# Kernel optimization log

Hardware: AMD Instinct MI355X
Metric: run time of the kernel (lower is better)

Reference implementation:

```python
import jax, jax.numpy as jnp
import numpy as np

DIM = 192
WIN = 7
HEADS = 6
SHIFT = 3
HID = 4 * DIM


def _ln(x, w, b, eps=1e-5):
    m = jnp.mean(x, axis=-1, keepdims=True)
    v = jnp.var(x, axis=-1, keepdims=True)
    return (x - m) * jax.lax.rsqrt(v + eps) * w + b


def setup_inputs() -> dict:
    key = jax.random.key(0)
    ks = jax.random.split(key, 8)
    B, C, H, W = 16, DIM, 56, 56
    s = lambda k, shape, fan: jax.random.normal(k, shape, jnp.float32) * (1.0 / np.sqrt(fan))
    return {
        "x": jax.random.normal(ks[0], (B, C, H, W), jnp.float32),
        "norm1_w": jnp.ones((C,), jnp.float32),
        "norm1_b": jnp.zeros((C,), jnp.float32),
        "qkv_w": s(ks[1], (3 * C, C), C),
        "qkv_b": jnp.zeros((3 * C,), jnp.float32),
        "proj_w": s(ks[2], (C, C), C),
        "proj_b": jnp.zeros((C,), jnp.float32),
        "norm2_w": jnp.ones((C,), jnp.float32),
        "norm2_b": jnp.zeros((C,), jnp.float32),
        "fc1_w": s(ks[3], (HID, C), C),
        "fc1_b": jnp.zeros((HID,), jnp.float32),
        "fc2_w": s(ks[4], (C, HID), HID),
        "fc2_b": jnp.zeros((C,), jnp.float32),
    }


def reference(x, norm1_w, norm1_b, qkv_w, qkv_b, proj_w, proj_b,
              norm2_w, norm2_b, fc1_w, fc1_b, fc2_w, fc2_b):
    B, C, H, W = x.shape
    shift = SHIFT if (H > WIN and W > WIN) else 0
    shortcut = x

    xl = jnp.transpose(x, (0, 2, 3, 1))            # B,H,W,C
    xl = _ln(xl, norm1_w, norm1_b)
    if shift > 0:
        xl = jnp.roll(xl, shift=(-shift, -shift), axis=(1, 2))
    nH, nW = H // WIN, W // WIN
    xw = xl.reshape(B, nH, WIN, nW, WIN, C)
    xw = jnp.transpose(xw, (0, 1, 3, 2, 4, 5)).reshape(-1, WIN * WIN, C)

    # window attention
    Bw, N, _ = xw.shape
    dh = C // HEADS
    qkv = jnp.einsum('bnc,oc->bno', xw, qkv_w) + qkv_b
    qkv = qkv.reshape(Bw, N, 3, HEADS, dh)
    q, k, v = qkv[:, :, 0], qkv[:, :, 1], qkv[:, :, 2]   # Bw,N,H,dh
    scale = dh ** -0.5
    attn = jnp.einsum('bnhd,bmhd->bhnm', q, k) * scale
    attn = jax.nn.softmax(attn, axis=-1)
    out = jnp.einsum('bhnm,bmhd->bnhd', attn, v).reshape(Bw, N, C)
    out = jnp.einsum('bnc,oc->bno', out, proj_w) + proj_b

    # window reverse -> B,H,W,C
    xl = out.reshape(B, nH, nW, WIN, WIN, C)
    xl = jnp.transpose(xl, (0, 1, 3, 2, 4, 5)).reshape(B, H, W, C)
    if shift > 0:
        xl = jnp.roll(xl, shift=(shift, shift), axis=(1, 2))

    # norm2 + MLP (note: original has NO attention residual)
    xl = _ln(xl, norm2_w, norm2_b)
    h = jnp.einsum('bhwc,oc->bhwo', xl, fc1_w) + fc1_b
    h = jax.nn.gelu(h, approximate=False)
    h = jnp.einsum('bhwo,co->bhwc', h, fc2_w) + fc2_b
    return jnp.transpose(h, (0, 3, 1, 2)) + shortcut
```

## Files before the change

### kernel.cpp

```cpp
#include <hip/hip_runtime.h>
#include <hip/hip_bf16.h>

typedef __bf16 bf16_t;
typedef __bf16 bf16x8 __attribute__((ext_vector_type(8)));
typedef float f32x4 __attribute__((ext_vector_type(4)));

#define MFMA16(a, b, c) __builtin_amdgcn_mfma_f32_16x16x32_bf16((a), (b), (c), 0, 0, 0)


__global__ __launch_bounds__(256) void k_cvt(const float* __restrict__ qkvw,
                                             const float* __restrict__ projw,
                                             const float* __restrict__ fc1w,
                                             const float* __restrict__ fc2w,
                                             bf16_t* __restrict__ dst)
{
    int i = blockIdx.x * 256 + threadIdx.x;
    if (i >= 442368) return;
    float v;
    if (i < 110592)      v = qkvw[i];
    else if (i < 147456) v = projw[i - 110592];
    else if (i < 294912) v = fc1w[i - 147456];
    else                 v = fc2w[i - 294912];
    dst[i] = (bf16_t)v;
}

__global__ __launch_bounds__(1024) void k_ln1(const float* __restrict__ x,
                                              const float* __restrict__ gam,
                                              const float* __restrict__ bet,
                                              bf16_t* __restrict__ xw)
{
    __shared__ float tile[56][193];
    __shared__ bf16_t obuf[56 * 192];
    const int bh = blockIdx.x;
    const int b = bh / 56, h = bh % 56;
    const int tid = threadIdx.x;

    {
        const int g = tid >> 4, u = tid & 15;
        const float* xb = x + (long)b * 602112 + (long)h * 56;
        if (u < 14) {
            #pragma unroll
            for (int k = 0; k < 3; ++k) {
                const int c = g + 64 * k;
                float4 v = *(const float4*)(xb + (long)c * 3136 + u * 4);
                tile[u * 4 + 0][c] = v.x;
                tile[u * 4 + 1][c] = v.y;
                tile[u * 4 + 2][c] = v.z;
                tile[u * 4 + 3][c] = v.w;
            }
        }
    }
    __syncthreads();

    const int wave = tid >> 6, lane = tid & 63;
    const float g0 = gam[lane], g1 = gam[lane + 64], g2 = gam[lane + 128];
    const float b0 = bet[lane], b1 = bet[lane + 64], b2 = bet[lane + 128];
    for (int wp = wave; wp < 56; wp += 16) {
        float v0 = tile[wp][lane], v1 = tile[wp][lane + 64], v2 = tile[wp][lane + 128];
        float s = v0 + v1 + v2;
        float sq = v0 * v0 + v1 * v1 + v2 * v2;
        #pragma unroll
        for (int d = 1; d < 64; d <<= 1) { s += __shfl_xor(s, d); sq += __shfl_xor(sq, d); }
        float mean = s * (1.f / 192.f);
        float var  = sq * (1.f / 192.f) - mean * mean;
        float rs = rsqrtf(var + 1e-5f);
        const int wr = (wp + 53) % 56;
        bf16_t* o = obuf + wr * 192;
        o[lane]       = (bf16_t)((v0 - mean) * rs * g0 + b0);
        o[lane + 64]  = (bf16_t)((v1 - mean) * rs * g1 + b1);
        o[lane + 128] = (bf16_t)((v2 - mean) * rs * g2 + b2);
    }
    __syncthreads();

    const int hr = (h + 53) % 56;
    const int nh = hr / 7, ii = hr % 7;
    const long rband = ((long)b * 64 + (long)nh * 8) * 49 + (long)ii * 7;
    const int4* src = (const int4*)obuf;
    for (int q = tid; q < 1344; q += 1024) {
        const int g = q / 168, u = q % 168;
        const int jj = u / 24, ci = u % 24;
        const long r = rband + (long)g * 49 + jj;
        ((int4*)xw)[r * 24 + ci] = src[(g * 7 + jj) * 24 + ci];
    }
}

template<int EPI>
__global__ __launch_bounds__(256) void k_gemm(const bf16_t* __restrict__ A,
                                              const bf16_t* __restrict__ W,
                                              const float* __restrict__ bias,
                                              void* __restrict__ outp,
                                              int M, int N, int K)
{
    __shared__ bf16_t As[128][72];
    __shared__ bf16_t Bs[64][72];
    const int tid = threadIdx.x;
    const int wave = tid >> 6, lane = tid & 63;
    const int lrow = lane & 15, lkg = lane >> 4;
    const int wm = (wave >> 1) * 64, wn = (wave & 1) * 32;
    const long m0 = (long)blockIdx.x * 128;
    const int n0 = blockIdx.y * 64;
    f32x4 acc[4][2];
    #pragma unroll
    for (int mi = 0; mi < 4; ++mi)
        #pragma unroll
        for (int ni = 0; ni < 2; ++ni)
            #pragma unroll
            for (int rg = 0; rg < 4; ++rg) acc[mi][ni][rg] = 0.f;

    for (int k0 = 0; k0 < K; k0 += 64) {
        #pragma unroll
        for (int it = 0; it < 4; ++it) {
            int e = (tid + it * 256) * 8;
            int r = e >> 6, c = e & 63;
            *(int4*)(&As[r][c]) = *(const int4*)(A + (m0 + r) * K + (k0 + c));
        }
        #pragma unroll
        for (int it = 0; it < 2; ++it) {
            int e = (tid + it * 256) * 8;
            int r = e >> 6, c = e & 63;
            *(int4*)(&Bs[r][c]) = *(const int4*)(W + (long)(n0 + r) * K + (k0 + c));
        }
        __syncthreads();
        #pragma unroll
        for (int kk = 0; kk < 64; kk += 32) {
            bf16x8 af[4], bfr[2];
            #pragma unroll
            for (int mi = 0; mi < 4; ++mi)
                af[mi] = *(const bf16x8*)(&As[wm + mi * 16 + lrow][kk + lkg * 8]);
            #pragma unroll
            for (int ni = 0; ni < 2; ++ni)
                bfr[ni] = *(const bf16x8*)(&Bs[wn + ni * 16 + lrow][kk + lkg * 8]);
            #pragma unroll
            for (int mi = 0; mi < 4; ++mi)
                #pragma unroll
                for (int ni = 0; ni < 2; ++ni)
                    acc[mi][ni] = MFMA16(af[mi], bfr[ni], acc[mi][ni]);
        }
        __syncthreads();
    }
    #pragma unroll
    for (int mi = 0; mi < 4; ++mi) {
        #pragma unroll
        for (int ni = 0; ni < 2; ++ni) {
            const int col = n0 + wn + ni * 16 + lrow;
            const float bv = bias[col];
            #pragma unroll
            for (int rg = 0; rg < 4; ++rg) {
                const long row = m0 + wm + mi * 16 + lkg * 4 + rg;
                float v = acc[mi][ni][rg] + bv;
                if (EPI == 2) v = 0.5f * v * (1.f + erff(v * 0.7071067811865475f));
                if (EPI == 1) ((float*)outp)[row * N + col] = v;
                else          ((bf16_t*)outp)[row * N + col] = (bf16_t)v;
            }
        }
    }
}

__global__ __launch_bounds__(64) void k_attn(const bf16_t* __restrict__ qkv,
                                             bf16_t* __restrict__ aout)
{
    __shared__ bf16_t Pl[64][72];
    __shared__ bf16_t Vt[32][72];
    const int win = blockIdx.x, head = blockIdx.y;
    const int lane = threadIdx.x;
    const int lrow = lane & 15, lkg = lane >> 4;
    const bf16_t* base = qkv + (long)win * 28224 + head * 32;

    {
        const int m = lane;
        const int mc = (m < 49) ? m : 48;
        const int4* vr = (const int4*)(base + (long)mc * 576 + 384);
        #pragma unroll
        for (int c4 = 0; c4 < 4; ++c4) {
            int4 vv = vr[c4];
            if (m >= 49) vv = make_int4(0, 0, 0, 0);
            const bf16_t* pe = (const bf16_t*)&vv;
            #pragma unroll
            for (int e = 0; e < 8; ++e) Vt[c4 * 8 + e][m] = pe[e];
        }
    }

    bf16x8 z8;
    #pragma unroll
    for (int e = 0; e < 8; ++e) z8[e] = (bf16_t)0.f;
    bf16x8 qf[4], kf[4];
    #pragma unroll
    for (int t = 0; t < 4; ++t) {
        const int n = t * 16 + lrow;
        const int nc = (n < 49) ? n : 48;
        bf16x8 qv = *(const bf16x8*)(base + (long)nc * 576 + lkg * 8);
        bf16x8 kv = *(const bf16x8*)(base + (long)nc * 576 + 192 + lkg * 8);
        qf[t] = (n < 49) ? qv : z8;
        kf[t] = (n < 49) ? kv : z8;
    }
    f32x4 zf; zf[0] = zf[1] = zf[2] = zf[3] = 0.f;
    f32x4 S[4][4];
    #pragma unroll
    for (int mi = 0; mi < 4; ++mi)
        #pragma unroll
        for (int mj = 0; mj < 4; ++mj)
            S[mi][mj] = MFMA16(qf[mi], kf[mj], zf);

    const float scl = 0.17677669529663687f;
    #pragma unroll
    for (int mi = 0; mi < 4; ++mi) {
        #pragma unroll
        for (int rg = 0; rg < 4; ++rg) {
            float v0 = S[mi][0][rg] * scl;
            float v1 = S[mi][1][rg] * scl;
            float v2 = S[mi][2][rg] * scl;
            float v3 = (lrow == 0) ? S[mi][3][rg] * scl : -1e30f;
            float mx = fmaxf(fmaxf(v0, v1), fmaxf(v2, v3));
            #pragma unroll
            for (int d = 1; d < 16; d <<= 1) mx = fmaxf(mx, __shfl_xor(mx, d));
            float e0 = expf(v0 - mx), e1 = expf(v1 - mx), e2 = expf(v2 - mx);
            float e3 = (lrow == 0) ? expf(v3 - mx) : 0.f;
            float sm = e0 + e1 + e2 + e3;
            #pragma unroll
            for (int d = 1; d < 16; d <<= 1) sm += __shfl_xor(sm, d);
            float is = 1.f / sm;
            const int row = mi * 16 + lkg * 4 + rg;
            Pl[row][lrow]      = (bf16_t)(e0 * is);
            Pl[row][16 + lrow] = (bf16_t)(e1 * is);
            Pl[row][32 + lrow] = (bf16_t)(e2 * is);
            Pl[row][48 + lrow] = (bf16_t)(e3 * is);
        }
    }
    __syncthreads();

    f32x4 o[4][2];
    #pragma unroll
    for (int ni = 0; ni < 4; ++ni)
        #pragma unroll
        for (int di = 0; di < 2; ++di)
            #pragma unroll
            for (int rg = 0; rg < 4; ++rg) o[ni][di][rg] = 0.f;
    #pragma unroll
    for (int m0 = 0; m0 < 64; m0 += 32) {
        bf16x8 pf[4], vf[2];
        #pragma unroll
        for (int ni = 0; ni < 4; ++ni)
            pf[ni] = *(const bf16x8*)(&Pl[ni * 16 + lrow][m0 + lkg * 8]);
        #pragma unroll
        for (int di = 0; di < 2; ++di)
            vf[di] = *(const bf16x8*)(&Vt[di * 16 + lrow][m0 + lkg * 8]);
        #pragma unroll
        for (int ni = 0; ni < 4; ++ni)
            #pragma unroll
            for (int di = 0; di < 2; ++di)
                o[ni][di] = MFMA16(pf[ni], vf[di], o[ni][di]);
    }
    #pragma unroll
    for (int ni = 0; ni < 4; ++ni) {
        #pragma unroll
        for (int rg = 0; rg < 4; ++rg) {
            const int n = ni * 16 + lkg * 4 + rg;
            if (n < 49) {
                bf16_t* orow = aout + ((long)win * 49 + n) * 192 + head * 32;
                orow[lrow]      = (bf16_t)o[ni][0][rg];
                orow[16 + lrow] = (bf16_t)o[ni][1][rg];
            }
        }
    }
}

__global__ __launch_bounds__(256) void k_ln2(const float* __restrict__ in,
                                             const float* __restrict__ gam,
                                             const float* __restrict__ bet,
                                             bf16_t* __restrict__ out)
{
    __shared__ bf16_t ob[4 * 192];
    const long row0 = (long)blockIdx.x * 4;
    const int wave = threadIdx.x >> 6, lane = threadIdx.x & 63;
    const float* r = in + (row0 + wave) * 192;
    float v0 = r[lane], v1 = r[lane + 64], v2 = r[lane + 128];
    float s = v0 + v1 + v2, sq = v0 * v0 + v1 * v1 + v2 * v2;
    #pragma unroll
    for (int d = 1; d < 64; d <<= 1) { s += __shfl_xor(s, d); sq += __shfl_xor(sq, d); }
    float mean = s * (1.f / 192.f);
    float var  = sq * (1.f / 192.f) - mean * mean;
    float rs = rsqrtf(var + 1e-5f);
    bf16_t* o = ob + wave * 192;
    o[lane]       = (bf16_t)((v0 - mean) * rs * gam[lane]       + bet[lane]);
    o[lane + 64]  = (bf16_t)((v1 - mean) * rs * gam[lane + 64]  + bet[lane + 64]);
    o[lane + 128] = (bf16_t)((v2 - mean) * rs * gam[lane + 128] + bet[lane + 128]);
    __syncthreads();
    if (threadIdx.x < 96)
        ((int4*)(out + row0 * 192))[threadIdx.x] = ((const int4*)ob)[threadIdx.x];
}

__global__ __launch_bounds__(1024) void k_final(const float* __restrict__ f,
                                                const float* __restrict__ x,
                                                float* __restrict__ out)
{
    __shared__ float tile[56][199];
    const int bh = blockIdx.x;
    const int b = bh / 56, hq = bh % 56;
    const int tid = threadIdx.x;
    const int hr = (hq + 53) % 56;
    const int nh = hr / 7, ii = hr % 7;
    const long rband = ((long)b * 64 + (long)nh * 8) * 49 + (long)ii * 7;

    for (int q = tid; q < 2688; q += 1024) {
        const int g = q / 336, rem = q % 336;
        const int jj = rem / 48, c4 = rem % 48;
        const long rr = rband + (long)g * 49 + jj;
        float4 v = *(const float4*)(f + rr * 192 + c4 * 4);
        const int wq = (g * 7 + jj + 3) % 56;
        tile[wq][c4 * 4 + 0] = v.x;
        tile[wq][c4 * 4 + 1] = v.y;
        tile[wq][c4 * 4 + 2] = v.z;
        tile[wq][c4 * 4 + 3] = v.w;
    }
    __syncthreads();

    const int g = tid >> 4, u = tid & 15;
    if (u < 14) {
        #pragma unroll
        for (int k = 0; k < 3; ++k) {
            const int c = g + 64 * k;
            const long base = ((long)b * 192 + c) * 3136 + (long)hq * 56 + u * 4;
            float4 xv = *(const float4*)(x + base);
            float4 ov;
            ov.x = tile[u * 4 + 0][c] + xv.x;
            ov.y = tile[u * 4 + 1][c] + xv.y;
            ov.z = tile[u * 4 + 2][c] + xv.z;
            ov.w = tile[u * 4 + 3][c] + xv.w;
            *(float4*)(out + base) = ov;
        }
    }
}

extern "C" void kernel_launch(void* const* d_in, const int* in_sizes, int n_in,
                              void* d_out, int out_size, void* d_ws, size_t ws_size,
                              hipStream_t stream)
{
    const float* x     = (const float*)d_in[0];
    const float* n1w   = (const float*)d_in[1];
    const float* n1b   = (const float*)d_in[2];
    const float* qkvw  = (const float*)d_in[3];
    const float* qkvb  = (const float*)d_in[4];
    const float* projw = (const float*)d_in[5];
    const float* projb = (const float*)d_in[6];
    const float* n2w   = (const float*)d_in[7];
    const float* n2b   = (const float*)d_in[8];
    const float* fc1w  = (const float*)d_in[9];
    const float* fc1b  = (const float*)d_in[10];
    const float* fc2w  = (const float*)d_in[11];
    const float* fc2b  = (const float*)d_in[12];

    char* ws = (char*)d_ws;
    bf16_t* wqkv  = (bf16_t*)(ws);
    bf16_t* wproj = (bf16_t*)(ws + 221184);
    bf16_t* wfc1  = (bf16_t*)(ws + 294912);
    bf16_t* wfc2  = (bf16_t*)(ws + 589824);
    bf16_t* Xb    = (bf16_t*)(ws + 884736);
    bf16_t* QKV   = (bf16_t*)(ws + 20152320);
    float*  F32B  = (float*) (ws + 77955072);
    bf16_t* Hb    = (bf16_t*)(ws + 116490240);

    k_cvt<<<1728, 256, 0, stream>>>(qkvw, projw, fc1w, fc2w, wqkv);
    k_ln1<<<896, 1024, 0, stream>>>(x, n1w, n1b, Xb);
    k_gemm<0><<<dim3(392, 9), 256, 0, stream>>>(Xb, wqkv, qkvb, QKV, 50176, 576, 192);
    k_attn<<<dim3(1024, 6), 64, 0, stream>>>(QKV, Xb);
    k_gemm<1><<<dim3(392, 3), 256, 0, stream>>>(Xb, wproj, projb, F32B, 50176, 192, 192);
    k_ln2<<<12544, 256, 0, stream>>>(F32B, n2w, n2b, Xb);
    k_gemm<2><<<dim3(392, 12), 256, 0, stream>>>(Xb, wfc1, fc1b, Hb, 50176, 768, 192);
    k_gemm<1><<<dim3(392, 3), 256, 0, stream>>>(Hb, wfc2, fc2b, F32B, 50176, 192, 768);
    k_final<<<896, 1024, 0, stream>>>(F32B, x, (float*)d_out);
}
```

Measured before the change: 209.0 us.

## Fuse proj GEMM with LayerNorm2, tanh-form GELU, bf16 fc2 output

```diff
diff --git a/kernel.cpp b/kernel.cpp
--- a/kernel.cpp
+++ b/kernel.cpp
@@ -148,9 +148,101 @@
             for (int rg = 0; rg < 4; ++rg) {
                 const long row = m0 + wm + mi * 16 + lkg * 4 + rg;
                 float v = acc[mi][ni][rg] + bv;
-                if (EPI == 2) v = 0.5f * v * (1.f + erff(v * 0.7071067811865475f));
-                if (EPI == 1) ((float*)outp)[row * N + col] = v;
-                else          ((bf16_t*)outp)[row * N + col] = (bf16_t)v;
+                if (EPI == 2) {
+                    float t2 = fminf(v * (1.5957691216057308f
+                                          + 0.07135481627f * v * v), 60.f);
+                    float e = __expf(t2);
+                    v = v * e / (e + 1.f);
+                }
+                ((bf16_t*)outp)[row * N + col] = (bf16_t)v;
+            }
+        }
+    }
+}
+
+__global__ __launch_bounds__(256) void k_proj_ln(const bf16_t* __restrict__ A,
+                                                 const bf16_t* __restrict__ W,
+                                                 const float* __restrict__ bias,
+                                                 const float* __restrict__ gam,
+                                                 const float* __restrict__ bet,
+                                                 bf16_t* __restrict__ out)
+{
+    __shared__ bf16_t As[128][72];
+    __shared__ bf16_t Bs[192][72];
+    const int tid = threadIdx.x;
+    const int wave = tid >> 6, lane = tid & 63;
+    const int lrow = lane & 15, lkg = lane >> 4;
+    const int wm = wave * 32;
+    const long m0 = (long)blockIdx.x * 128;
+
+    f32x4 acc[2][12];
+    #pragma unroll
+    for (int mi = 0; mi < 2; ++mi)
+        #pragma unroll
+        for (int ni = 0; ni < 12; ++ni)
+            #pragma unroll
+            for (int rg = 0; rg < 4; ++rg) acc[mi][ni][rg] = 0.f;
+
+    for (int k0 = 0; k0 < 192; k0 += 64) {
+        #pragma unroll
+        for (int it = 0; it < 4; ++it) {
+            int e = (tid + it * 256) * 8;
+            int r = e >> 6, c = e & 63;
+            *(int4*)(&As[r][c]) = *(const int4*)(A + (m0 + r) * 192 + (k0 + c));
+        }
+        #pragma unroll
+        for (int it = 0; it < 6; ++it) {
+            int e = (tid + it * 256) * 8;
+            int r = e >> 6, c = e & 63;
+            *(int4*)(&Bs[r][c]) = *(const int4*)(W + (long)r * 192 + (k0 + c));
+        }
+        __syncthreads();
+        #pragma unroll
+        for (int kk = 0; kk < 64; kk += 32) {
+            bf16x8 af[2];
+            #pragma unroll
+            for (int mi = 0; mi < 2; ++mi)
+                af[mi] = *(const bf16x8*)(&As[wm + mi * 16 + lrow][kk + lkg * 8]);
+            #pragma unroll
+            for (int ni = 0; ni < 12; ++ni) {
+                bf16x8 bfr = *(const bf16x8*)(&Bs[ni * 16 + lrow][kk + lkg * 8]);
+                acc[0][ni] = MFMA16(af[0], bfr, acc[0][ni]);
+                acc[1][ni] = MFMA16(af[1], bfr, acc[1][ni]);
+            }
+        }
+        __syncthreads();
+    }
+
+    float bv[12];
+    #pragma unroll
+    for (int ni = 0; ni < 12; ++ni) bv[ni] = bias[ni * 16 + lrow];
+
+    #pragma unroll
+    for (int mi = 0; mi < 2; ++mi) {
+        #pragma unroll
+        for (int rg = 0; rg < 4; ++rg) {
+            float val[12];
+            float s = 0.f, sq = 0.f;
+            #pragma unroll
+            for (int ni = 0; ni < 12; ++ni) {
+                val[ni] = acc[mi][ni][rg] + bv[ni];
+                s += val[ni];
+                sq += val[ni] * val[ni];
+            }
+            #pragma unroll
+            for (int d = 1; d < 16; d <<= 1) {
+                s += __shfl_xor(s, d);
+                sq += __shfl_xor(sq, d);
+            }
+            float mean = s * (1.f / 192.f);
+            float var  = sq * (1.f / 192.f) - mean * mean;
+            float rs = rsqrtf(var + 1e-5f);
+            const long row = m0 + wm + mi * 16 + lkg * 4 + rg;
+            bf16_t* orow = out + row * 192;
+            #pragma unroll
+            for (int ni = 0; ni < 12; ++ni) {
+                const int col = ni * 16 + lrow;
+                orow[col] = (bf16_t)((val[ni] - mean) * rs * gam[col] + bet[col]);
             }
         }
     }
@@ -264,32 +356,7 @@
     }
 }
 
-__global__ __launch_bounds__(256) void k_ln2(const float* __restrict__ in,
-                                             const float* __restrict__ gam,
-                                             const float* __restrict__ bet,
-                                             bf16_t* __restrict__ out)
-{
-    __shared__ bf16_t ob[4 * 192];
-    const long row0 = (long)blockIdx.x * 4;
-    const int wave = threadIdx.x >> 6, lane = threadIdx.x & 63;
-    const float* r = in + (row0 + wave) * 192;
-    float v0 = r[lane], v1 = r[lane + 64], v2 = r[lane + 128];
-    float s = v0 + v1 + v2, sq = v0 * v0 + v1 * v1 + v2 * v2;
-    #pragma unroll
-    for (int d = 1; d < 64; d <<= 1) { s += __shfl_xor(s, d); sq += __shfl_xor(sq, d); }
-    float mean = s * (1.f / 192.f);
-    float var  = sq * (1.f / 192.f) - mean * mean;
-    float rs = rsqrtf(var + 1e-5f);
-    bf16_t* o = ob + wave * 192;
-    o[lane]       = (bf16_t)((v0 - mean) * rs * gam[lane]       + bet[lane]);
-    o[lane + 64]  = (bf16_t)((v1 - mean) * rs * gam[lane + 64]  + bet[lane + 64]);
-    o[lane + 128] = (bf16_t)((v2 - mean) * rs * gam[lane + 128] + bet[lane + 128]);
-    __syncthreads();
-    if (threadIdx.x < 96)
-        ((int4*)(out + row0 * 192))[threadIdx.x] = ((const int4*)ob)[threadIdx.x];
-}
-
-__global__ __launch_bounds__(1024) void k_final(const float* __restrict__ f,
+__global__ __launch_bounds__(1024) void k_final(const bf16_t* __restrict__ fb,
                                                 const float* __restrict__ x,
                                                 float* __restrict__ out)
 {
@@ -301,16 +368,14 @@
     const int nh = hr / 7, ii = hr % 7;
     const long rband = ((long)b * 64 + (long)nh * 8) * 49 + (long)ii * 7;
 
-    for (int q = tid; q < 2688; q += 1024) {
-        const int g = q / 336, rem = q % 336;
-        const int jj = rem / 48, c4 = rem % 48;
+    for (int q = tid; q < 1344; q += 1024) {
+        const int g = q / 168, rem = q % 168;
+        const int jj = rem / 24, ci = rem % 24;
         const long rr = rband + (long)g * 49 + jj;
-        float4 v = *(const float4*)(f + rr * 192 + c4 * 4);
+        bf16x8 v = *(const bf16x8*)(fb + rr * 192 + ci * 8);
         const int wq = (g * 7 + jj + 3) % 56;
-        tile[wq][c4 * 4 + 0] = v.x;
-        tile[wq][c4 * 4 + 1] = v.y;
-        tile[wq][c4 * 4 + 2] = v.z;
-        tile[wq][c4 * 4 + 3] = v.w;
+        #pragma unroll
+        for (int e = 0; e < 8; ++e) tile[wq][ci * 8 + e] = (float)v[e];
     }
     __syncthreads();
 
@@ -356,16 +421,16 @@
     bf16_t* wfc2  = (bf16_t*)(ws + 589824);
     bf16_t* Xb    = (bf16_t*)(ws + 884736);
     bf16_t* QKV   = (bf16_t*)(ws + 20152320);
-    float*  F32B  = (float*) (ws + 77955072);
-    bf16_t* Hb    = (bf16_t*)(ws + 116490240);
+    bf16_t* Hb    = (bf16_t*)(ws + 77955072);
+    bf16_t* H2    = (bf16_t*)(ws + 155025408);
+    bf16_t* X2    = (bf16_t*)(ws + 174292992);
 
     k_cvt<<<1728, 256, 0, stream>>>(qkvw, projw, fc1w, fc2w, wqkv);
     k_ln1<<<896, 1024, 0, stream>>>(x, n1w, n1b, Xb);
     k_gemm<0><<<dim3(392, 9), 256, 0, stream>>>(Xb, wqkv, qkvb, QKV, 50176, 576, 192);
     k_attn<<<dim3(1024, 6), 64, 0, stream>>>(QKV, Xb);
-    k_gemm<1><<<dim3(392, 3), 256, 0, stream>>>(Xb, wproj, projb, F32B, 50176, 192, 192);
-    k_ln2<<<12544, 256, 0, stream>>>(F32B, n2w, n2b, Xb);
-    k_gemm<2><<<dim3(392, 12), 256, 0, stream>>>(Xb, wfc1, fc1b, Hb, 50176, 768, 192);
-    k_gemm<1><<<dim3(392, 3), 256, 0, stream>>>(Hb, wfc2, fc2b, F32B, 50176, 192, 768);
-    k_final<<<896, 1024, 0, stream>>>(F32B, x, (float*)d_out);
-}
+    k_proj_ln<<<392, 256, 0, stream>>>(Xb, wproj, projb, n2w, n2b, X2);
+    k_gemm<2><<<dim3(392, 12), 256, 0, stream>>>(X2, wfc1, fc1b, Hb, 50176, 768, 192);
+    k_gemm<0><<<dim3(392, 3), 256, 0, stream>>>(Hb, wfc2, fc2b, H2, 50176, 192, 768);
+    k_final<<<896, 1024, 0, stream>>>(H2, x, (float*)d_out);
+}
```

Result: slower. 215.8 us (+3.3%).
